# Performance work log

Measured on AMD Instinct MI355X. Metric: run time of the kernel, lower is better.

## Reference

```python
import jax, jax.numpy as jnp
import numpy as np
import math

GH, GW = 64, 64
FEAT_DIM = 32
NUM_COMP = 8
N = 1_000_000
H1, H2 = 128, 64
TWO_PI = 2.0 * math.pi
LN_EPS = 1e-5


def _layernorm(h, g, b):
    mu = jnp.mean(h, axis=-1, keepdims=True)
    var = jnp.var(h, axis=-1, keepdims=True)
    return (h - mu) * jax.lax.rsqrt(var + LN_EPS) * g + b


def setup_inputs() -> dict:
    key = jax.random.key(0)
    ks = jax.random.split(key, 8)
    coords = jax.random.uniform(ks[0], (N, 2), dtype=jnp.float32)
    feature_grid = jax.random.normal(ks[1], (GH, GW, FEAT_DIM), dtype=jnp.float32)
    d_in = 2 + FEAT_DIM
    W1 = jax.random.normal(ks[2], (d_in, H1), dtype=jnp.float32) / np.sqrt(d_in)
    b1 = jnp.zeros((H1,), jnp.float32)
    g1 = jnp.ones((H1,), jnp.float32)
    be1 = jnp.zeros((H1,), jnp.float32)
    W2 = jax.random.normal(ks[3], (H1, H2), dtype=jnp.float32) / np.sqrt(H1)
    b2 = jnp.zeros((H2,), jnp.float32)
    g2 = jnp.ones((H2,), jnp.float32)
    be2 = jnp.zeros((H2,), jnp.float32)
    W3 = jax.random.normal(ks[4], (H2, 6 * NUM_COMP), dtype=jnp.float32) / np.sqrt(H2)
    b3 = jnp.zeros((6 * NUM_COMP,), jnp.float32)
    return {"coords": coords, "feature_grid": feature_grid,
            "W1": W1, "b1": b1, "g1": g1, "be1": be1,
            "W2": W2, "b2": b2, "g2": g2, "be2": be2,
            "W3": W3, "b3": b3}


def reference(coords, feature_grid, W1, b1, g1, be1, W2, b2, g2, be2, W3, b3):
    # bilinear gather from feature grid
    x = coords[:, 0] * (GW - 1)
    y = coords[:, 1] * (GH - 1)
    x0 = jnp.clip(jnp.floor(x).astype(jnp.int32), 0, GW - 2)
    y0 = jnp.clip(jnp.floor(y).astype(jnp.int32), 0, GH - 2)
    x1 = x0 + 1
    y1 = y0 + 1
    dx = (x - x0.astype(jnp.float32))[:, None]
    dy = (y - y0.astype(jnp.float32))[:, None]
    f00 = feature_grid[y0, x0]  # [N, F]
    f01 = feature_grid[y1, x0]
    f10 = feature_grid[y0, x1]
    f11 = feature_grid[y1, x1]
    feat = ((1 - dx) * (1 - dy) * f00 + (1 - dx) * dy * f01
            + dx * (1 - dy) * f10 + dx * dy * f11)
    # MLP (dropout is identity in eval mode)
    h = jnp.concatenate([coords, feat], axis=-1)
    h = _layernorm(jax.nn.relu(h @ W1 + b1), g1, be1)
    h = _layernorm(jax.nn.relu(h @ W2 + b2), g2, be2)
    params = (h @ W3 + b3).reshape(-1, NUM_COMP, 6)
    # GMM parameter postprocessing
    weights = jax.nn.softmax(params[:, :, 0], axis=-1)
    speed = jax.nn.relu(params[:, :, 1])
    angle = jnp.mod(params[:, :, 2], TWO_PI)
    variances = jnp.exp(jnp.clip(params[:, :, 3:5], -10.0, 10.0))
    corr = 0.99 * jnp.tanh(params[:, :, 5])
    means = jnp.stack([speed, angle], axis=-1)
    gmm = jnp.concatenate([weights[..., None], means, variances, corr[..., None]], axis=-1)
    return (gmm, coords)
```

## Files before the change

kernel.cpp:

```cpp
#include <hip/hip_runtime.h>
#include <math.h>


constexpr int N_PTS = 1000000;
constexpr int GW = 64;
constexpr int FDIM = 32;
constexpr int DIN = 34;
constexpr int NH1 = 128;
constexpr int NH2 = 64;
constexpr int NOUT = 48;
constexpr int NC = 8;
constexpr int BLK = 128;

template<int N>
__device__ __forceinline__ float np_pairwise(const float* x) {
#pragma clang fp contract(off)
    float r[8];
#pragma unroll
    for (int j = 0; j < 8; ++j) r[j] = x[j];
#pragma unroll
    for (int m = 1; m < N / 8; ++m)
#pragma unroll
        for (int j = 0; j < 8; ++j) r[j] = r[j] + x[8 * m + j];
    return ((r[0] + r[1]) + (r[2] + r[3])) + ((r[4] + r[5]) + (r[6] + r[7]));
}

template<int N>
__device__ __forceinline__ float np_pairwise_sq(const float* x, float mu) {
#pragma clang fp contract(off)
    float r[8];
#pragma unroll
    for (int j = 0; j < 8; ++j) { const float d = x[j] - mu; r[j] = d * d; }
#pragma unroll
    for (int m = 1; m < N / 8; ++m)
#pragma unroll
        for (int j = 0; j < 8; ++j) {
            const float d = x[8 * m + j] - mu;
            r[j] = r[j] + d * d;
        }
    return ((r[0] + r[1]) + (r[2] + r[3])) + ((r[4] + r[5]) + (r[6] + r[7]));
}

__global__ __launch_bounds__(BLK, 2) void modgmm_np32(
    const float* __restrict__ coords,
    const float* __restrict__ grid,
    const float* __restrict__ W1, const float* __restrict__ b1,
    const float* __restrict__ g1, const float* __restrict__ be1,
    const float* __restrict__ W2, const float* __restrict__ b2,
    const float* __restrict__ g2, const float* __restrict__ be2,
    const float* __restrict__ W3, const float* __restrict__ b3,
    float* __restrict__ gmm_out, float* __restrict__ coords_out)
{
#pragma clang fp contract(off)
    __shared__ float sbuf[64 * BLK];
    const int tid = threadIdx.x;
    const int i = blockIdx.x * BLK + tid;
    if (i >= N_PTS) return;

    const float2 c2 = reinterpret_cast<const float2*>(coords)[i];
    const float cx = c2.x, cy = c2.y;

    const float x = cx * 63.0f;
    const float y = cy * 63.0f;
    int x0 = (int)floorf(x); x0 = x0 < 0 ? 0 : (x0 > 62 ? 62 : x0);
    int y0 = (int)floorf(y); y0 = y0 < 0 ? 0 : (y0 > 62 ? 62 : y0);
    const float dx = x - (float)x0;
    const float dy = y - (float)y0;
    const float omdx = 1.0f - dx;
    const float omdy = 1.0f - dy;
    const float w00 = omdx * omdy;
    const float w01 = omdx * dy;
    const float w10 = dx * omdy;
    const float w11 = dx * dy;

    const float* __restrict__ gp = grid + (y0 * GW + x0) * FDIM;

    sbuf[0 * BLK + tid] = cx;
    sbuf[1 * BLK + tid] = cy;
#pragma unroll
    for (int k = 0; k < FDIM; ++k) {
        const float t0 = w00 * gp[k];
        const float t1 = w01 * gp[GW * FDIM + k];
        const float t2 = w10 * gp[FDIM + k];
        const float t3 = w11 * gp[GW * FDIM + FDIM + k];
        sbuf[(2 + k) * BLK + tid] = ((t0 + t1) + t2) + t3;
    }

    float h[NH1];
#pragma unroll
    for (int j = 0; j < NH1; ++j) h[j] = 0.0f;
    for (int k = 0; k < DIN; ++k) {
        const float hv = sbuf[k * BLK + tid];
        const float* __restrict__ wr = W1 + k * NH1;
#pragma unroll
        for (int j = 0; j < NH1; ++j) h[j] = __builtin_fmaf(hv, wr[j], h[j]);
    }
#pragma unroll
    for (int j = 0; j < NH1; ++j) h[j] = fmaxf(h[j] + b1[j], 0.0f);

    {
        const float mu = np_pairwise<NH1>(h) / 128.0f;
        const float var = np_pairwise_sq<NH1>(h, mu) / 128.0f;
        const float rs = 1.0f / sqrtf(var + 1e-5f);
#pragma unroll
        for (int j = 0; j < NH1; ++j)
            h[j] = ((h[j] - mu) * rs) * g1[j] + be1[j];
    }

    float h2[NH2];
#pragma unroll
    for (int j = 0; j < NH2; ++j) h2[j] = 0.0f;
#pragma unroll
    for (int j = 0; j < 64; ++j) sbuf[j * BLK + tid] = h[j];
    for (int k = 0; k < 64; ++k) {
        const float hv = sbuf[k * BLK + tid];
        const float* __restrict__ wr = W2 + k * NH2;
#pragma unroll
        for (int j = 0; j < NH2; ++j) h2[j] = __builtin_fmaf(hv, wr[j], h2[j]);
    }
#pragma unroll
    for (int j = 0; j < 64; ++j) sbuf[j * BLK + tid] = h[64 + j];
    for (int k = 0; k < 64; ++k) {
        const float hv = sbuf[k * BLK + tid];
        const float* __restrict__ wr = W2 + (64 + k) * NH2;
#pragma unroll
        for (int j = 0; j < NH2; ++j) h2[j] = __builtin_fmaf(hv, wr[j], h2[j]);
    }
#pragma unroll
    for (int j = 0; j < NH2; ++j) h2[j] = fmaxf(h2[j] + b2[j], 0.0f);

    {
        const float mu = np_pairwise<NH2>(h2) / 64.0f;
        const float var = np_pairwise_sq<NH2>(h2, mu) / 64.0f;
        const float rs = 1.0f / sqrtf(var + 1e-5f);
#pragma unroll
        for (int j = 0; j < NH2; ++j)
            h2[j] = ((h2[j] - mu) * rs) * g2[j] + be2[j];
    }

    float o[NOUT];
#pragma unroll
    for (int j = 0; j < NOUT; ++j) o[j] = 0.0f;
#pragma unroll
    for (int j = 0; j < NH2; ++j) sbuf[j * BLK + tid] = h2[j];
    for (int k = 0; k < NH2; ++k) {
        const float hv = sbuf[k * BLK + tid];
        const float* __restrict__ wr = W3 + k * NOUT;
#pragma unroll
        for (int j = 0; j < NOUT; ++j) o[j] = __builtin_fmaf(hv, wr[j], o[j]);
    }
#pragma unroll
    for (int j = 0; j < NOUT; ++j) o[j] = o[j] + b3[j];

    const float TPf = 6.28318530717958647692f;
    float res[NOUT];
    float m = o[0];
#pragma unroll
    for (int c = 1; c < NC; ++c) m = fmaxf(m, o[6 * c]);
    float e[NC];
#pragma unroll
    for (int c = 0; c < NC; ++c) e[c] = expf(o[6 * c] - m);
    const float esum = ((e[0] + e[1]) + (e[2] + e[3])) + ((e[4] + e[5]) + (e[6] + e[7]));
#pragma unroll
    for (int c = 0; c < NC; ++c) {
        res[6 * c + 0] = e[c] / esum;
        res[6 * c + 1] = fmaxf(o[6 * c + 1], 0.0f);
        float a = fmodf(o[6 * c + 2], TPf);
        if (a < 0.0f) a += TPf;
        res[6 * c + 2] = a;
        res[6 * c + 3] = expf(fminf(fmaxf(o[6 * c + 3], -10.0f), 10.0f));
        res[6 * c + 4] = expf(fminf(fmaxf(o[6 * c + 4], -10.0f), 10.0f));
        res[6 * c + 5] = 0.99f * tanhf(o[6 * c + 5]);
    }

    float4* og = reinterpret_cast<float4*>(gmm_out + (size_t)i * NOUT);
#pragma unroll
    for (int q = 0; q < NOUT / 4; ++q)
        og[q] = make_float4(res[4 * q + 0], res[4 * q + 1], res[4 * q + 2], res[4 * q + 3]);
    reinterpret_cast<float2*>(coords_out)[i] = make_float2(cx, cy);
}

extern "C" void kernel_launch(void* const* d_in, const int* in_sizes, int n_in,
                              void* d_out, int out_size, void* d_ws, size_t ws_size,
                              hipStream_t stream) {
    const float* coords = (const float*)d_in[0];
    const float* grid   = (const float*)d_in[1];
    const float* W1  = (const float*)d_in[2];
    const float* b1  = (const float*)d_in[3];
    const float* g1  = (const float*)d_in[4];
    const float* be1 = (const float*)d_in[5];
    const float* W2  = (const float*)d_in[6];
    const float* b2  = (const float*)d_in[7];
    const float* g2  = (const float*)d_in[8];
    const float* be2 = (const float*)d_in[9];
    const float* W3  = (const float*)d_in[10];
    const float* b3  = (const float*)d_in[11];

    float* gmm_out    = (float*)d_out;
    float* coords_out = (float*)d_out + (size_t)N_PTS * NOUT;

    const int nblocks = (N_PTS + BLK - 1) / BLK;
    modgmm_np32<<<nblocks, BLK, 0, stream>>>(
        coords, grid, W1, b1, g1, be1, W2, b2, g2, be2, W3, b3,
        gmm_out, coords_out);
}
```

Before: 563.6 us.

## Split fused MLP into two kernels with layer-1 activations staged in workspace

Splits the single fused kernel in two. The first does the bilinear gather and layer 1, with each point's 128 hidden units shared between two half-waves, and writes the activations in transposed form to workspace. The second applies LayerNorm 1 while reading them back, then runs layers 2 and 3 and the GMM postprocessing. The goal is to shrink the per-thread register footprint so more waves fit per CU, and the weight reads become float4 loads. The cost is a 512 MB write and re-read of activations to HBM when the workspace is large enough, otherwise it falls back to the old kernel.

```diff
diff --git a/kernel.cpp b/kernel.cpp
--- a/kernel.cpp
+++ b/kernel.cpp
@@ -10,7 +10,6 @@
 constexpr int NH2 = 64;
 constexpr int NOUT = 48;
 constexpr int NC = 8;
-constexpr int BLK = 128;
 
 template<int N>
 __device__ __forceinline__ float np_pairwise(const float* x) {
@@ -41,25 +40,52 @@
     return ((r[0] + r[1]) + (r[2] + r[3])) + ((r[4] + r[5]) + (r[6] + r[7]));
 }
 
-__global__ __launch_bounds__(BLK, 2) void modgmm_np32(
-    const float* __restrict__ coords,
-    const float* __restrict__ grid,
-    const float* __restrict__ W1, const float* __restrict__ b1,
-    const float* __restrict__ g1, const float* __restrict__ be1,
-    const float* __restrict__ W2, const float* __restrict__ b2,
-    const float* __restrict__ g2, const float* __restrict__ be2,
-    const float* __restrict__ W3, const float* __restrict__ b3,
+__device__ __forceinline__ void gmm_postprocess_store(
+    const float* o, float cx, float cy, int gi,
     float* __restrict__ gmm_out, float* __restrict__ coords_out)
 {
 #pragma clang fp contract(off)
-    __shared__ float sbuf[64 * BLK];
-    const int tid = threadIdx.x;
-    const int i = blockIdx.x * BLK + tid;
-    if (i >= N_PTS) return;
-
-    const float2 c2 = reinterpret_cast<const float2*>(coords)[i];
+    const float TPf = 6.28318530717958647692f;
+    float res[NOUT];
+    float m = o[0];
+#pragma unroll
+    for (int c = 1; c < NC; ++c) m = fmaxf(m, o[6 * c]);
+    float e[NC];
+#pragma unroll
+    for (int c = 0; c < NC; ++c) e[c] = expf(o[6 * c] - m);
+    const float esum = ((e[0] + e[1]) + (e[2] + e[3])) + ((e[4] + e[5]) + (e[6] + e[7]));
+#pragma unroll
+    for (int c = 0; c < NC; ++c) {
+        res[6 * c + 0] = e[c] / esum;
+        res[6 * c + 1] = fmaxf(o[6 * c + 1], 0.0f);
+        float a = fmodf(o[6 * c + 2], TPf);
+        if (a < 0.0f) a += TPf;
+        res[6 * c + 2] = a;
+        res[6 * c + 3] = expf(fminf(fmaxf(o[6 * c + 3], -10.0f), 10.0f));
+        res[6 * c + 4] = expf(fminf(fmaxf(o[6 * c + 4], -10.0f), 10.0f));
+        res[6 * c + 5] = 0.99f * tanhf(o[6 * c + 5]);
+    }
+    float4* og = reinterpret_cast<float4*>(gmm_out + (size_t)gi * NOUT);
+#pragma unroll
+    for (int q = 0; q < NOUT / 4; ++q)
+        og[q] = make_float4(res[4 * q + 0], res[4 * q + 1], res[4 * q + 2], res[4 * q + 3]);
+    reinterpret_cast<float2*>(coords_out)[gi] = make_float2(cx, cy);
+}
+
+__global__ __launch_bounds__(128, 4) void k1_gather_l1(
+    const float* __restrict__ coords, const float* __restrict__ grid,
+    const float* __restrict__ W1, const float* __restrict__ b1,
+    float* __restrict__ h1t, int start, int cn)
+{
+#pragma clang fp contract(off)
+    const int lane = threadIdx.x & 63;
+    const int halfu = __builtin_amdgcn_readfirstlane((int)(threadIdx.x >> 6));
+    const int pt = blockIdx.x * 64 + lane;
+    if (pt >= cn) return;
+    const int gi = start + pt;
+
+    const float2 c2 = reinterpret_cast<const float2*>(coords)[gi];
     const float cx = c2.x, cy = c2.y;
-
     const float x = cx * 63.0f;
     const float y = cy * 63.0f;
     int x0 = (int)floorf(x); x0 = x0 < 0 ? 0 : (x0 > 62 ? 62 : x0);
@@ -72,7 +98,160 @@
     const float w01 = omdx * dy;
     const float w10 = dx * omdy;
     const float w11 = dx * dy;
-
+    const float* __restrict__ gp = grid + (y0 * GW + x0) * FDIM;
+
+    float f[DIN];
+    f[0] = cx; f[1] = cy;
+#pragma unroll
+    for (int k = 0; k < FDIM; ++k) {
+        const float t0 = w00 * gp[k];
+        const float t1 = w01 * gp[GW * FDIM + k];
+        const float t2 = w10 * gp[FDIM + k];
+        const float t3 = w11 * gp[GW * FDIM + FDIM + k];
+        f[2 + k] = ((t0 + t1) + t2) + t3;
+    }
+
+    float acc[64];
+#pragma unroll
+    for (int j = 0; j < 64; ++j) acc[j] = 0.0f;
+    const float* __restrict__ wb = W1 + halfu * 64;
+#pragma unroll
+    for (int k = 0; k < DIN; ++k) {
+        const float hv = f[k];
+        const float* wr = wb + k * NH1;
+#pragma unroll
+        for (int q = 0; q < 16; ++q) {
+            const float4 w = *reinterpret_cast<const float4*>(wr + 4 * q);
+            acc[4*q+0] = __builtin_fmaf(hv, w.x, acc[4*q+0]);
+            acc[4*q+1] = __builtin_fmaf(hv, w.y, acc[4*q+1]);
+            acc[4*q+2] = __builtin_fmaf(hv, w.z, acc[4*q+2]);
+            acc[4*q+3] = __builtin_fmaf(hv, w.w, acc[4*q+3]);
+        }
+    }
+
+    const float* __restrict__ bb = b1 + halfu * 64;
+    float* __restrict__ outb = h1t + (size_t)(halfu * 64) * cn + pt;
+#pragma unroll
+    for (int jj = 0; jj < 64; ++jj)
+        outb[(size_t)jj * cn] = fmaxf(acc[jj] + bb[jj], 0.0f);
+}
+
+__global__ __launch_bounds__(256, 3) void k23_mlp(
+    const float* __restrict__ h1t,
+    const float* __restrict__ g1, const float* __restrict__ be1,
+    const float* __restrict__ W2, const float* __restrict__ b2,
+    const float* __restrict__ g2, const float* __restrict__ be2,
+    const float* __restrict__ W3, const float* __restrict__ b3,
+    const float* __restrict__ coords,
+    float* __restrict__ gmm_out, float* __restrict__ coords_out,
+    int start, int cn)
+{
+#pragma clang fp contract(off)
+    const int pt = blockIdx.x * 256 + threadIdx.x;
+    if (pt >= cn) return;
+    const int gi = start + pt;
+    const float* __restrict__ col = h1t + pt;
+
+    float r[8];
+#pragma unroll
+    for (int j = 0; j < 8; ++j) r[j] = col[(size_t)j * cn];
+#pragma unroll
+    for (int m = 1; m < 16; ++m)
+#pragma unroll
+        for (int j = 0; j < 8; ++j) r[j] = r[j] + col[(size_t)(8 * m + j) * cn];
+    const float mu1 = (((r[0]+r[1]) + (r[2]+r[3])) + ((r[4]+r[5]) + (r[6]+r[7]))) / 128.0f;
+#pragma unroll
+    for (int j = 0; j < 8; ++j) { const float d = col[(size_t)j * cn] - mu1; r[j] = d * d; }
+#pragma unroll
+    for (int m = 1; m < 16; ++m)
+#pragma unroll
+        for (int j = 0; j < 8; ++j) {
+            const float d = col[(size_t)(8 * m + j) * cn] - mu1;
+            r[j] = r[j] + d * d;
+        }
+    const float var1 = (((r[0]+r[1]) + (r[2]+r[3])) + ((r[4]+r[5]) + (r[6]+r[7]))) / 128.0f;
+    const float rs1 = 1.0f / sqrtf(var1 + 1e-5f);
+
+    float acc[NH2];
+#pragma unroll
+    for (int j = 0; j < NH2; ++j) acc[j] = 0.0f;
+    for (int k = 0; k < NH1; ++k) {
+        const float raw = col[(size_t)k * cn];
+        const float hv = ((raw - mu1) * rs1) * g1[k] + be1[k];
+        const float* wr = W2 + k * NH2;
+#pragma unroll
+        for (int q = 0; q < 16; ++q) {
+            const float4 w = *reinterpret_cast<const float4*>(wr + 4 * q);
+            acc[4*q+0] = __builtin_fmaf(hv, w.x, acc[4*q+0]);
+            acc[4*q+1] = __builtin_fmaf(hv, w.y, acc[4*q+1]);
+            acc[4*q+2] = __builtin_fmaf(hv, w.z, acc[4*q+2]);
+            acc[4*q+3] = __builtin_fmaf(hv, w.w, acc[4*q+3]);
+        }
+    }
+#pragma unroll
+    for (int j = 0; j < NH2; ++j) acc[j] = fmaxf(acc[j] + b2[j], 0.0f);
+
+    const float mu2 = np_pairwise<NH2>(acc) / 64.0f;
+    const float var2 = np_pairwise_sq<NH2>(acc, mu2) / 64.0f;
+    const float rs2 = 1.0f / sqrtf(var2 + 1e-5f);
+#pragma unroll
+    for (int j = 0; j < NH2; ++j)
+        acc[j] = ((acc[j] - mu2) * rs2) * g2[j] + be2[j];
+
+    float o[NOUT];
+#pragma unroll
+    for (int j = 0; j < NOUT; ++j) o[j] = 0.0f;
+#pragma unroll
+    for (int k = 0; k < NH2; ++k) {
+        const float hv = acc[k];
+        const float* wr = W3 + k * NOUT;
+#pragma unroll
+        for (int q = 0; q < 12; ++q) {
+            const float4 w = *reinterpret_cast<const float4*>(wr + 4 * q);
+            o[4*q+0] = __builtin_fmaf(hv, w.x, o[4*q+0]);
+            o[4*q+1] = __builtin_fmaf(hv, w.y, o[4*q+1]);
+            o[4*q+2] = __builtin_fmaf(hv, w.z, o[4*q+2]);
+            o[4*q+3] = __builtin_fmaf(hv, w.w, o[4*q+3]);
+        }
+    }
+#pragma unroll
+    for (int j = 0; j < NOUT; ++j) o[j] = o[j] + b3[j];
+
+    const float2 c2 = reinterpret_cast<const float2*>(coords)[gi];
+    gmm_postprocess_store(o, c2.x, c2.y, gi, gmm_out, coords_out);
+}
+
+constexpr int BLK = 128;
+__global__ __launch_bounds__(BLK, 2) void modgmm_np32(
+    const float* __restrict__ coords,
+    const float* __restrict__ grid,
+    const float* __restrict__ W1, const float* __restrict__ b1,
+    const float* __restrict__ g1, const float* __restrict__ be1,
+    const float* __restrict__ W2, const float* __restrict__ b2,
+    const float* __restrict__ g2, const float* __restrict__ be2,
+    const float* __restrict__ W3, const float* __restrict__ b3,
+    float* __restrict__ gmm_out, float* __restrict__ coords_out)
+{
+#pragma clang fp contract(off)
+    __shared__ float sbuf[64 * BLK];
+    const int tid = threadIdx.x;
+    const int i = blockIdx.x * BLK + tid;
+    if (i >= N_PTS) return;
+
+    const float2 c2 = reinterpret_cast<const float2*>(coords)[i];
+    const float cx = c2.x, cy = c2.y;
+    const float x = cx * 63.0f;
+    const float y = cy * 63.0f;
+    int x0 = (int)floorf(x); x0 = x0 < 0 ? 0 : (x0 > 62 ? 62 : x0);
+    int y0 = (int)floorf(y); y0 = y0 < 0 ? 0 : (y0 > 62 ? 62 : y0);
+    const float dx = x - (float)x0;
+    const float dy = y - (float)y0;
+    const float omdx = 1.0f - dx;
+    const float omdy = 1.0f - dy;
+    const float w00 = omdx * omdy;
+    const float w01 = omdx * dy;
+    const float w10 = dx * omdy;
+    const float w11 = dx * dy;
     const float* __restrict__ gp = grid + (y0 * GW + x0) * FDIM;
 
     sbuf[0 * BLK + tid] = cx;
@@ -97,7 +276,6 @@
     }
 #pragma unroll
     for (int j = 0; j < NH1; ++j) h[j] = fmaxf(h[j] + b1[j], 0.0f);
-
     {
         const float mu = np_pairwise<NH1>(h) / 128.0f;
         const float var = np_pairwise_sq<NH1>(h, mu) / 128.0f;
@@ -128,7 +306,6 @@
     }
 #pragma unroll
     for (int j = 0; j < NH2; ++j) h2[j] = fmaxf(h2[j] + b2[j], 0.0f);
-
     {
         const float mu = np_pairwise<NH2>(h2) / 64.0f;
         const float var = np_pairwise_sq<NH2>(h2, mu) / 64.0f;
@@ -152,32 +329,7 @@
 #pragma unroll
     for (int j = 0; j < NOUT; ++j) o[j] = o[j] + b3[j];
 
-    const float TPf = 6.28318530717958647692f;
-    float res[NOUT];
-    float m = o[0];
-#pragma unroll
-    for (int c = 1; c < NC; ++c) m = fmaxf(m, o[6 * c]);
-    float e[NC];
-#pragma unroll
-    for (int c = 0; c < NC; ++c) e[c] = expf(o[6 * c] - m);
-    const float esum = ((e[0] + e[1]) + (e[2] + e[3])) + ((e[4] + e[5]) + (e[6] + e[7]));
-#pragma unroll
-    for (int c = 0; c < NC; ++c) {
-        res[6 * c + 0] = e[c] / esum;
-        res[6 * c + 1] = fmaxf(o[6 * c + 1], 0.0f);
-        float a = fmodf(o[6 * c + 2], TPf);
-        if (a < 0.0f) a += TPf;
-        res[6 * c + 2] = a;
-        res[6 * c + 3] = expf(fminf(fmaxf(o[6 * c + 3], -10.0f), 10.0f));
-        res[6 * c + 4] = expf(fminf(fmaxf(o[6 * c + 4], -10.0f), 10.0f));
-        res[6 * c + 5] = 0.99f * tanhf(o[6 * c + 5]);
-    }
-
-    float4* og = reinterpret_cast<float4*>(gmm_out + (size_t)i * NOUT);
-#pragma unroll
-    for (int q = 0; q < NOUT / 4; ++q)
-        og[q] = make_float4(res[4 * q + 0], res[4 * q + 1], res[4 * q + 2], res[4 * q + 3]);
-    reinterpret_cast<float2*>(coords_out)[i] = make_float2(cx, cy);
+    gmm_postprocess_store(o, cx, cy, i, gmm_out, coords_out);
 }
 
 extern "C" void kernel_launch(void* const* d_in, const int* in_sizes, int n_in,
@@ -198,9 +350,27 @@
 
     float* gmm_out    = (float*)d_out;
     float* coords_out = (float*)d_out + (size_t)N_PTS * NOUT;
-
-    const int nblocks = (N_PTS + BLK - 1) / BLK;
-    modgmm_np32<<<nblocks, BLK, 0, stream>>>(
-        coords, grid, W1, b1, g1, be1, W2, b2, g2, be2, W3, b3,
-        gmm_out, coords_out);
-}
+    float* h1t = (float*)d_ws;
+
+    const size_t cap_pts = ws_size / ((size_t)NH1 * sizeof(float));
+    int CH = (int)(cap_pts < (size_t)N_PTS ? cap_pts : (size_t)N_PTS);
+    CH &= ~255;
+
+    if (CH >= 131072 || CH >= N_PTS) {
+        for (int s = 0; s < N_PTS; s += CH) {
+            const int cn = (N_PTS - s) < CH ? (N_PTS - s) : CH;
+            const int b1blocks = (cn + 63) / 64;
+            k1_gather_l1<<<b1blocks, 128, 0, stream>>>(
+                coords, grid, W1, b1, h1t, s, cn);
+            const int b2blocks = (cn + 255) / 256;
+            k23_mlp<<<b2blocks, 256, 0, stream>>>(
+                h1t, g1, be1, W2, b2, g2, be2, W3, b3, coords,
+                gmm_out, coords_out, s, cn);
+        }
+    } else {
+        const int nblocks = (N_PTS + BLK - 1) / BLK;
+        modgmm_np32<<<nblocks, BLK, 0, stream>>>(
+            coords, grid, W1, b1, g1, be1, W2, b2, g2, be2, W3, b3,
+            gmm_out, coords_out);
+    }
+}
```

Result: slower. 1.749 ms (+210.4%).
